# Kernel tuning notes

Measured on AMD Instinct MI355X. Metric: run time of the kernel, lower is better.

The kernel has to match this reference:

```python
import jax, jax.numpy as jnp
import numpy as np

INPUT_SIZE = 256
HIDDEN_SIZE = 128
OUTPUT_SIZE = 16
N_NODES = 100000
N_EDGES = 1600000


def setup_inputs() -> dict:
    key = jax.random.key(0)
    k_x, k_e, k_w, k_bc, k_wl, k_bl = jax.random.split(key, 6)
    x = jax.random.normal(k_x, (N_NODES, INPUT_SIZE), dtype=jnp.float32)
    edge_index = jax.random.randint(k_e, (2, N_EDGES), 0, N_NODES, dtype=jnp.int64)
    # GCNConv params: lin weight (no bias inside lin), bias added after aggregation
    s1 = 1.0 / np.sqrt(INPUT_SIZE)
    W_conv = jax.random.uniform(k_w, (INPUT_SIZE, HIDDEN_SIZE), jnp.float32, -s1, s1)
    b_conv = jnp.zeros((HIDDEN_SIZE,), jnp.float32)
    s2 = 1.0 / np.sqrt(HIDDEN_SIZE)
    W_lin = jax.random.uniform(k_wl, (HIDDEN_SIZE, OUTPUT_SIZE), jnp.float32, -s2, s2)
    b_lin = jax.random.uniform(k_bl, (OUTPUT_SIZE,), jnp.float32, -s2, s2)
    return {"x": x, "edge_index": edge_index, "W_conv": W_conv, "b_conv": b_conv,
            "W_lin": W_lin, "b_lin": b_lin}


def reference(x, edge_index, W_conv, b_conv, W_lin, b_lin):
    N = x.shape[0]
    # GCNConv: add self-loops, symmetric degree normalization, scatter-add aggregation
    loop = jnp.arange(N, dtype=edge_index.dtype)
    src = jnp.concatenate([edge_index[0], loop])  # [E+N]
    dst = jnp.concatenate([edge_index[1], loop])  # [E+N]
    deg = jax.ops.segment_sum(jnp.ones_like(dst, dtype=x.dtype), dst, num_segments=N)
    dinv = jnp.where(deg > 0, jax.lax.rsqrt(deg), 0.0)
    norm = dinv[src] * dinv[dst]  # [E+N]
    h = x @ W_conv  # [N, H] transform before propagation (as in PyG GCNConv)
    msgs = h[src] * norm[:, None]  # [E+N, H] gathered messages
    agg = jax.ops.segment_sum(msgs, dst, num_segments=N) + b_conv  # [N, H]
    h = jax.nn.relu(agg)
    # dropout is identity in eval mode
    logits = h @ W_lin + b_lin  # [N, C]
    return jax.nn.log_softmax(logits, axis=1)
```

## Files before the change

kernel.cpp:

```cpp
#include <hip/hip_runtime.h>
#include <math.h>

#define NN    100000
#define INF_  256
#define HID   128
#define OUTF  16
#define NE    1600000
#define BUK   256
#define NBUK  ((NN + BUK - 1) / BUK)
#define NB_F  128
#define EPB_F (NE / NB_F)
#define NB2   (NBUK * NB_F)
#define WPREP_B 128
#define GEMM_B ((NN + 127) / 128)
#define GBLK  3125
#define NPW   8

typedef __attribute__((ext_vector_type(4))) float f32x4;
typedef __attribute__((ext_vector_type(8))) short bf16x8;

__device__ inline unsigned short f32_to_bf16(float f) {
  union { float f; unsigned int u; } v; v.f = f;
  unsigned int x = v.u;
  unsigned int r = x + 0x7fffu + ((x >> 16) & 1u);
  return (unsigned short)(r >> 16);
}
__device__ inline unsigned pack_bf16(float f0, float f1) {
  return (unsigned)f32_to_bf16(f0) | ((unsigned)f32_to_bf16(f1) << 16);
}
__device__ inline float bf16lo_to_f32(unsigned int u) {
  union { unsigned int u; float f; } v; v.u = u << 16; return v.f;
}
__device__ inline float bf16hi_to_f32(unsigned int u) {
  union { unsigned int u; float f; } v; v.u = u & 0xffff0000u; return v.f;
}

#define ACC_FP8(u, acc) do { \
  acc[0] += __builtin_amdgcn_cvt_f32_fp8((u).x, 0); \
  acc[1] += __builtin_amdgcn_cvt_f32_fp8((u).x, 1); \
  acc[2] += __builtin_amdgcn_cvt_f32_fp8((u).x, 2); \
  acc[3] += __builtin_amdgcn_cvt_f32_fp8((u).x, 3); \
  acc[4] += __builtin_amdgcn_cvt_f32_fp8((u).y, 0); \
  acc[5] += __builtin_amdgcn_cvt_f32_fp8((u).y, 1); \
  acc[6] += __builtin_amdgcn_cvt_f32_fp8((u).y, 2); \
  acc[7] += __builtin_amdgcn_cvt_f32_fp8((u).y, 3); \
} while (0)

__global__ __launch_bounds__(256) void k_pre(const int* __restrict__ dst,
                                             int* __restrict__ H,
                                             const float* __restrict__ W,
                                             unsigned short* __restrict__ WTs) {
  __shared__ int lh[NBUK];
  const int t = threadIdx.x;
  if (blockIdx.x < NB_F) {
    const int b = blockIdx.x;
    for (int i = t; i < NBUK; i += 256) lh[i] = 0;
    __syncthreads();
    const int beg = b * EPB_F;
    for (int i = beg + t; i < beg + EPB_F; i += 256) atomicAdd(&lh[dst[i] >> 8], 1);
    __syncthreads();
    for (int i = t; i < NBUK; i += 256) H[i * NB_F + b] = lh[i];
  } else {
    const int i = (blockIdx.x - NB_F) * 256 + t;
    if (i < INF_ * HID) {
      const int k = i >> 7, n = i & 127;
      const int s = k >> 5, c = (k >> 3) & 3, j = k & 7;
      const int chunk = s * 512 + n * 4 + (c ^ (n & 3));
      WTs[chunk * 8 + j] = f32_to_bf16(W[i]);
    }
  }
}

__global__ __launch_bounds__(256) void k_fillb(const int* __restrict__ src,
                                               const int* __restrict__ dst,
                                               const int* __restrict__ H,
                                               int* __restrict__ gB,
                                               unsigned int* __restrict__ binned) {
  __shared__ int lbase[NBUK];
  __shared__ int lcnt[NBUK];
  __shared__ int tot[NBUK];
  __shared__ int bb[NBUK + 1];
  __shared__ int sh[256];
  const int t = threadIdx.x;
  const int myblk = blockIdx.x;

#pragma unroll
  for (int rr = 0; rr < 2; ++rr) {
    const int i = t + rr * 256;
    if (i < NBUK) {
      const int* row = &H[i * NB_F];
      int pre = 0, tt = 0;
      for (int k = 0; k < NB_F; ++k) {
        const int h = row[k];
        tt += h;
        if (k < myblk) pre += h;
      }
      tot[i] = tt; lbase[i] = pre; lcnt[i] = 0;
    }
  }
  __syncthreads();
  const int i0 = 2 * t, i1 = 2 * t + 1;
  const int va = (i0 < NBUK) ? tot[i0] : 0;
  const int vb = (i1 < NBUK) ? tot[i1] : 0;
  sh[t] = va + vb;
  __syncthreads();
  for (int off = 1; off < 256; off <<= 1) {
    int tmp = (t >= off) ? sh[t - off] : 0;
    __syncthreads();
    sh[t] += tmp;
    __syncthreads();
  }
  int run = (t > 0) ? sh[t - 1] : 0;
  if (i0 < NBUK) bb[i0] = run;
  if (i1 < NBUK) bb[i1] = run + va;
  if (t == 255) bb[NBUK] = run + va + vb;
  __syncthreads();
#pragma unroll
  for (int rr = 0; rr < 2; ++rr) {
    const int i = t + rr * 256;
    if (i < NBUK) {
      lbase[i] += bb[i];
      if (myblk == 0) gB[i] = bb[i];
    }
  }
  if (myblk == 0 && t == 0) gB[NBUK] = bb[NBUK];
  __syncthreads();

  const int beg = myblk * EPB_F;
#pragma unroll 4
  for (int i = beg + t; i < beg + EPB_F; i += 256) {
    const int d = dst[i];
    const int b = d >> 8;
    const unsigned w = ((unsigned)src[i] << 8) | (unsigned)(d & 255);
    const int pos = atomicAdd(&lcnt[b], 1);
    binned[lbase[b] + pos] = w;
  }
}

__global__ __launch_bounds__(256) void k_csr(const unsigned int* __restrict__ binned,
                                             const int* __restrict__ gB,
                                             int* __restrict__ rowptr,
                                             float* __restrict__ dinv,
                                             int* __restrict__ csr) {
  __shared__ int hist[BUK];
  __shared__ int sh[256];
  __shared__ int lcur[BUK];
  const int b = blockIdx.x, t = threadIdx.x;
  hist[t] = 0;
  __syncthreads();
  const int e0 = gB[b], e1 = gB[b + 1];
  for (int i = e0 + t; i < e1; i += 256) atomicAdd(&hist[binned[i] & 255u], 1);
  __syncthreads();
  const int hv = hist[t];
  sh[t] = hv;
  __syncthreads();
  for (int off = 1; off < 256; off <<= 1) {
    int tmp = (t >= off) ? sh[t - off] : 0;
    __syncthreads();
    sh[t] += tmp;
    __syncthreads();
  }
  const int excl = sh[t] - hv;
  lcur[t] = excl;
  const int nid = b * BUK + t;
  if (nid < NN) {
    rowptr[nid] = e0 + excl;
    dinv[nid] = rsqrtf((float)(hv + 1));
  }
  if (b == NBUK - 1 && t == 0) rowptr[NN] = e1;
  __syncthreads();
  for (int i = e0 + t; i < e1; i += 256) {
    const unsigned w = binned[i];
    const int pos = atomicAdd(&lcur[w & 255u], 1);
    csr[e0 + pos] = (int)(w >> 8);
  }
}

__global__ __launch_bounds__(256) void k_gemm(const float* __restrict__ x,
                                              const unsigned short* __restrict__ WTs,
                                              const float* __restrict__ dinv,
                                              uint4* __restrict__ h2b4,
                                              uint2* __restrict__ h8) {
  __shared__ unsigned short xs[128 * 32];
  __shared__ unsigned short ws[128 * 32];
  const int tid = threadIdx.x;
  const int wave = tid >> 6, lane = tid & 63;
  const int l15 = lane & 15, l4 = lane >> 4;
  const int row0 = blockIdx.x * 128;

  f32x4 acc[2][8];
#pragma unroll
  for (int rb = 0; rb < 2; ++rb)
#pragma unroll
    for (int n = 0; n < 8; ++n) { acc[rb][n].x = 0.f; acc[rb][n].y = 0.f; acc[rb][n].z = 0.f; acc[rb][n].w = 0.f; }

  for (int s = 0; s < 8; ++s) {
#pragma unroll
    for (int p = 0; p < 2; ++p) {
      const int c = tid + p * 256;
      const int row = c >> 2, kc = c & 3;
      const int grow = row0 + row;
      unsigned short tmp[8];
      if (grow < NN) {
        const float4 v0 = *(const float4*)&x[(size_t)grow * INF_ + s * 32 + kc * 8];
        const float4 v1 = *(const float4*)&x[(size_t)grow * INF_ + s * 32 + kc * 8 + 4];
        tmp[0] = f32_to_bf16(v0.x); tmp[1] = f32_to_bf16(v0.y);
        tmp[2] = f32_to_bf16(v0.z); tmp[3] = f32_to_bf16(v0.w);
        tmp[4] = f32_to_bf16(v1.x); tmp[5] = f32_to_bf16(v1.y);
        tmp[6] = f32_to_bf16(v1.z); tmp[7] = f32_to_bf16(v1.w);
      } else {
#pragma unroll
        for (int j = 0; j < 8; ++j) tmp[j] = 0;
      }
      const int phys = kc ^ (row & 3);
      *(bf16x8*)&xs[(row * 4 + phys) * 8] = *(bf16x8*)tmp;
    }
#pragma unroll
    for (int p = 0; p < 2; ++p) {
      const int c = tid + p * 256;
      *(bf16x8*)&ws[c * 8] = *(const bf16x8*)&WTs[(s * 512 + c) * 8];
    }
    __syncthreads();
    bf16x8 af[2];
#pragma unroll
    for (int rb = 0; rb < 2; ++rb) {
      const int row = wave * 32 + rb * 16 + l15;
      af[rb] = *(const bf16x8*)&xs[(row * 4 + (l4 ^ (row & 3))) * 8];
    }
#pragma unroll
    for (int n = 0; n < 8; ++n) {
      const int col = n * 16 + l15;
      const bf16x8 bf = *(const bf16x8*)&ws[(col * 4 + (l4 ^ (col & 3))) * 8];
      acc[0][n] = __builtin_amdgcn_mfma_f32_16x16x32_bf16(af[0], bf, acc[0][n], 0, 0, 0);
      acc[1][n] = __builtin_amdgcn_mfma_f32_16x16x32_bf16(af[1], bf, acc[1][n], 0, 0, 0);
    }
    __syncthreads();
  }
#pragma unroll
  for (int rb = 0; rb < 2; ++rb) {
#pragma unroll
    for (int r = 0; r < 4; ++r) {
      const int rowg = row0 + wave * 32 + rb * 16 + l4 * 4 + r;
      if (rowg < NN) {
        const float dv = dinv[rowg];
        float vv[8];
#pragma unroll
        for (int n = 0; n < 8; ++n) vv[n] = acc[rb][n][r] * dv;
        uint4 o4;
        o4.x = pack_bf16(vv[0], vv[1]);
        o4.y = pack_bf16(vv[2], vv[3]);
        o4.z = pack_bf16(vv[4], vv[5]);
        o4.w = pack_bf16(vv[6], vv[7]);
        h2b4[(size_t)rowg * 16 + l15] = o4;
        int a0 = 0, a1 = 0;
        a0 = __builtin_amdgcn_cvt_pk_fp8_f32(vv[0], vv[1], a0, false);
        a0 = __builtin_amdgcn_cvt_pk_fp8_f32(vv[2], vv[3], a0, true);
        a1 = __builtin_amdgcn_cvt_pk_fp8_f32(vv[4], vv[5], a1, false);
        a1 = __builtin_amdgcn_cvt_pk_fp8_f32(vv[6], vv[7], a1, true);
        h8[(size_t)rowg * 16 + l15] = make_uint2((unsigned)a0, (unsigned)a1);
      }
    }
  }
}

__global__ __launch_bounds__(256) void k_gather(const int* __restrict__ rowptr,
                                                const int* __restrict__ csr,
                                                const uint2* __restrict__ h8p,
                                                const uint4* __restrict__ h2b4,
                                                const float* __restrict__ dinv,
                                                const float* __restrict__ bc,
                                                const float* __restrict__ Wl,
                                                const float* __restrict__ bl,
                                                float* __restrict__ out) {
  const int lane = threadIdx.x & 63;
  const int m = lane & 15, eg = lane >> 4;
  const int wid = __builtin_amdgcn_readfirstlane(blockIdx.x * 4 + (threadIdx.x >> 6));
  const int v0 = wid * NPW;
  if (v0 >= NN) return;
  const int v1 = min(v0 + NPW, NN);

  float4 wl[8];
#pragma unroll
  for (int r = 0; r < 8; ++r) wl[r] = *(const float4*)&Wl[(size_t)(16 * r + m) * OUTF + 4 * eg];
  float bcj[8];
#pragma unroll
  for (int j = 0; j < 8; ++j) bcj[j] = bc[16 * j + m];
  const float4 bl4 = *(const float4*)&bl[4 * eg];

  for (int v = v0; v < v1; ++v) {
    const int rp = __builtin_amdgcn_readfirstlane(rowptr[v]);
    const int re = __builtin_amdgcn_readfirstlane(rowptr[v + 1]);
    float acc[8];
#pragma unroll
    for (int q = 0; q < 8; ++q) acc[q] = 0.f;

    for (int base = rp; base < re; base += 64) {
      const int nb = min(64, re - base);
      const int csrv = (base + lane < re) ? csr[base + lane] : 0;
      int o = 0;
      for (; o + 32 <= nb; o += 32) {
        const int s0 = __shfl(csrv, o + eg);
        const int s1 = __shfl(csrv, o + 4 + eg);
        const int s2 = __shfl(csrv, o + 8 + eg);
        const int s3 = __shfl(csrv, o + 12 + eg);
        const int s4 = __shfl(csrv, o + 16 + eg);
        const int s5 = __shfl(csrv, o + 20 + eg);
        const int s6 = __shfl(csrv, o + 24 + eg);
        const int s7 = __shfl(csrv, o + 28 + eg);
        const uint2 u0 = h8p[(size_t)s0 * 16 + m];
        const uint2 u1 = h8p[(size_t)s1 * 16 + m];
        const uint2 u2 = h8p[(size_t)s2 * 16 + m];
        const uint2 u3 = h8p[(size_t)s3 * 16 + m];
        const uint2 u4 = h8p[(size_t)s4 * 16 + m];
        const uint2 u5 = h8p[(size_t)s5 * 16 + m];
        const uint2 u6 = h8p[(size_t)s6 * 16 + m];
        const uint2 u7 = h8p[(size_t)s7 * 16 + m];
        ACC_FP8(u0, acc); ACC_FP8(u1, acc); ACC_FP8(u2, acc); ACC_FP8(u3, acc);
        ACC_FP8(u4, acc); ACC_FP8(u5, acc); ACC_FP8(u6, acc); ACC_FP8(u7, acc);
      }
      for (; o + 16 <= nb; o += 16) {
        const int s0 = __shfl(csrv, o + eg);
        const int s1 = __shfl(csrv, o + 4 + eg);
        const int s2 = __shfl(csrv, o + 8 + eg);
        const int s3 = __shfl(csrv, o + 12 + eg);
        const uint2 u0 = h8p[(size_t)s0 * 16 + m];
        const uint2 u1 = h8p[(size_t)s1 * 16 + m];
        const uint2 u2 = h8p[(size_t)s2 * 16 + m];
        const uint2 u3 = h8p[(size_t)s3 * 16 + m];
        ACC_FP8(u0, acc); ACC_FP8(u1, acc); ACC_FP8(u2, acc); ACC_FP8(u3, acc);
      }
      for (; o < nb; o += 4) {
        const int src = __shfl(csrv, o + eg);
        if (o + eg < nb) {
          const uint2 u = h8p[(size_t)src * 16 + m];
          ACC_FP8(u, acc);
        }
      }
    }
#pragma unroll
    for (int q = 0; q < 8; ++q) {
      acc[q] += __shfl_xor(acc[q], 16);
      acc[q] += __shfl_xor(acc[q], 32);
    }
    const float dv = dinv[v];
    const uint4 su = h2b4[(size_t)v * 16 + m];
    float t[8];
    t[0] = fmaxf(fmaf(dv, acc[0] + bf16lo_to_f32(su.x), bcj[0]), 0.f);
    t[1] = fmaxf(fmaf(dv, acc[1] + bf16hi_to_f32(su.x), bcj[1]), 0.f);
    t[2] = fmaxf(fmaf(dv, acc[2] + bf16lo_to_f32(su.y), bcj[2]), 0.f);
    t[3] = fmaxf(fmaf(dv, acc[3] + bf16hi_to_f32(su.y), bcj[3]), 0.f);
    t[4] = fmaxf(fmaf(dv, acc[4] + bf16lo_to_f32(su.z), bcj[4]), 0.f);
    t[5] = fmaxf(fmaf(dv, acc[5] + bf16hi_to_f32(su.z), bcj[5]), 0.f);
    t[6] = fmaxf(fmaf(dv, acc[6] + bf16lo_to_f32(su.w), bcj[6]), 0.f);
    t[7] = fmaxf(fmaf(dv, acc[7] + bf16hi_to_f32(su.w), bcj[7]), 0.f);
    float p0 = 0.f, p1 = 0.f, p2 = 0.f, p3 = 0.f;
#pragma unroll
    for (int r = 0; r < 8; ++r) {
      p0 = fmaf(t[r], wl[r].x, p0);
      p1 = fmaf(t[r], wl[r].y, p1);
      p2 = fmaf(t[r], wl[r].z, p2);
      p3 = fmaf(t[r], wl[r].w, p3);
    }
#pragma unroll
    for (int off = 1; off <= 8; off <<= 1) {
      p0 += __shfl_xor(p0, off);
      p1 += __shfl_xor(p1, off);
      p2 += __shfl_xor(p2, off);
      p3 += __shfl_xor(p3, off);
    }
    p0 += bl4.x; p1 += bl4.y; p2 += bl4.z; p3 += bl4.w;
    float mx = fmaxf(fmaxf(p0, p1), fmaxf(p2, p3));
    mx = fmaxf(mx, __shfl_xor(mx, 16));
    mx = fmaxf(mx, __shfl_xor(mx, 32));
    float se = expf(p0 - mx) + expf(p1 - mx) + expf(p2 - mx) + expf(p3 - mx);
    se += __shfl_xor(se, 16);
    se += __shfl_xor(se, 32);
    const float lse = mx + logf(se);
    if (m == 0) {
      float4 o4;
      o4.x = p0 - lse; o4.y = p1 - lse; o4.z = p2 - lse; o4.w = p3 - lse;
      *(float4*)&out[(size_t)v * OUTF + 4 * eg] = o4;
    }
  }
}

extern "C" void kernel_launch(void* const* d_in, const int* in_sizes, int n_in,
                              void* d_out, int out_size, void* d_ws, size_t ws_size,
                              hipStream_t stream) {
  const float* x  = (const float*)d_in[0];
  const int*   ei = (const int*)d_in[1];
  const float* Wc = (const float*)d_in[2];
  const float* bc = (const float*)d_in[3];
  const float* Wl = (const float*)d_in[4];
  const float* bl = (const float*)d_in[5];
  float* out = (float*)d_out;

  uint4* h2b4 = (uint4*)d_ws;
  unsigned short* WTs = (unsigned short*)(h2b4 + (size_t)NN * 16);
  float* dinv   = (float*)(WTs + (size_t)INF_ * HID);
  int*   rowptr = (int*)(dinv + NN);
  int*   H      = rowptr + NN + 1;
  int*   gB     = H + NB2;
  unsigned int* binned = (unsigned int*)(gB + NBUK + 1);
  int*   csr    = (int*)(binned + NE);
  uint2* h8     = (uint2*)(csr + NE);

  const int* srcv = ei;
  const int* dstv = ei + NE;

  k_pre<<<NB_F + WPREP_B, 256, 0, stream>>>(dstv, H, Wc, WTs);
  k_fillb<<<NB_F, 256, 0, stream>>>(srcv, dstv, H, gB, binned);
  k_csr<<<NBUK, 256, 0, stream>>>(binned, gB, rowptr, dinv, csr);
  k_gemm<<<GEMM_B, 256, 0, stream>>>(x, WTs, dinv, h2b4, h8);
  k_gather<<<GBLK, 256, 0, stream>>>(rowptr, csr, h8, h2b4, dinv, bc, Wl, bl, out);
}
```

Baseline: 196.5 us.

## Split FP8 feature table into column slices for cache-resident gather, add merge kernel

The GEMM now writes the FP8 hidden features as four 32-column slices stored as separate planes. Each slice is 3.2MB and can stay resident in L2/LLC while blocks mapped to that slice gather from it. The gather kernel is restructured so each block handles one slice and writes fp32 partial sums to a workspace. A new merge kernel applies the normalization, bias, ReLU, the small linear layer and log-softmax through shared memory. The self-loop term now uses the FP8 value instead of the bf16 copy, which lowers precision slightly. The change adds a 51MB fp32 intermediate write and read plus one extra kernel launch, in exchange for better cache locality of the random gathers.

```diff
diff --git a/kernel.cpp b/kernel.cpp
--- a/kernel.cpp
+++ b/kernel.cpp
@@ -13,8 +13,8 @@
 #define NB2   (NBUK * NB_F)
 #define WPREP_B 128
 #define GEMM_B ((NN + 127) / 128)
-#define GBLK  3125
-#define NPW   8
+#define NRANGE ((NN + 63) / 64)
+#define GW_BLOCKS 2048
 
 typedef __attribute__((ext_vector_type(4))) float f32x4;
 typedef __attribute__((ext_vector_type(8))) short bf16x8;
@@ -25,26 +25,19 @@
   unsigned int r = x + 0x7fffu + ((x >> 16) & 1u);
   return (unsigned short)(r >> 16);
 }
-__device__ inline unsigned pack_bf16(float f0, float f1) {
-  return (unsigned)f32_to_bf16(f0) | ((unsigned)f32_to_bf16(f1) << 16);
-}
-__device__ inline float bf16lo_to_f32(unsigned int u) {
-  union { unsigned int u; float f; } v; v.u = u << 16; return v.f;
-}
-__device__ inline float bf16hi_to_f32(unsigned int u) {
-  union { unsigned int u; float f; } v; v.u = u & 0xffff0000u; return v.f;
-}
-
-#define ACC_FP8(u, acc) do { \
-  acc[0] += __builtin_amdgcn_cvt_f32_fp8((u).x, 0); \
-  acc[1] += __builtin_amdgcn_cvt_f32_fp8((u).x, 1); \
-  acc[2] += __builtin_amdgcn_cvt_f32_fp8((u).x, 2); \
-  acc[3] += __builtin_amdgcn_cvt_f32_fp8((u).x, 3); \
-  acc[4] += __builtin_amdgcn_cvt_f32_fp8((u).y, 0); \
-  acc[5] += __builtin_amdgcn_cvt_f32_fp8((u).y, 1); \
-  acc[6] += __builtin_amdgcn_cvt_f32_fp8((u).y, 2); \
-  acc[7] += __builtin_amdgcn_cvt_f32_fp8((u).y, 3); \
+
+#define ACC4(u) do { \
+  a0 += __builtin_amdgcn_cvt_f32_fp8((u), 0); \
+  a1 += __builtin_amdgcn_cvt_f32_fp8((u), 1); \
+  a2 += __builtin_amdgcn_cvt_f32_fp8((u), 2); \
+  a3 += __builtin_amdgcn_cvt_f32_fp8((u), 3); \
 } while (0)
+
+__device__ inline int chmap(int c_lin) {
+  const int s = c_lin >> 5, g = (c_lin >> 2) & 7, k = c_lin & 3;
+  const int kk = (k == 0) ? 0 : (k == 1) ? 16 : (k == 2) ? 1 : 17;
+  return 32 * s + 2 * g + kk;
+}
 
 __global__ __launch_bounds__(256) void k_pre(const int* __restrict__ dst,
                                              int* __restrict__ H,
@@ -179,8 +172,7 @@
 __global__ __launch_bounds__(256) void k_gemm(const float* __restrict__ x,
                                               const unsigned short* __restrict__ WTs,
                                               const float* __restrict__ dinv,
-                                              uint4* __restrict__ h2b4,
-                                              uint2* __restrict__ h8) {
+                                              unsigned short* __restrict__ h8q) {
   __shared__ unsigned short xs[128 * 32];
   __shared__ unsigned short ws[128 * 32];
   const int tid = threadIdx.x;
@@ -246,141 +238,147 @@
         float vv[8];
 #pragma unroll
         for (int n = 0; n < 8; ++n) vv[n] = acc[rb][n][r] * dv;
-        uint4 o4;
-        o4.x = pack_bf16(vv[0], vv[1]);
-        o4.y = pack_bf16(vv[2], vv[3]);
-        o4.z = pack_bf16(vv[4], vv[5]);
-        o4.w = pack_bf16(vv[6], vv[7]);
-        h2b4[(size_t)rowg * 16 + l15] = o4;
-        int a0 = 0, a1 = 0;
-        a0 = __builtin_amdgcn_cvt_pk_fp8_f32(vv[0], vv[1], a0, false);
-        a0 = __builtin_amdgcn_cvt_pk_fp8_f32(vv[2], vv[3], a0, true);
-        a1 = __builtin_amdgcn_cvt_pk_fp8_f32(vv[4], vv[5], a1, false);
-        a1 = __builtin_amdgcn_cvt_pk_fp8_f32(vv[6], vv[7], a1, true);
-        h8[(size_t)rowg * 16 + l15] = make_uint2((unsigned)a0, (unsigned)a1);
-      }
-    }
-  }
-}
-
-__global__ __launch_bounds__(256) void k_gather(const int* __restrict__ rowptr,
-                                                const int* __restrict__ csr,
-                                                const uint2* __restrict__ h8p,
-                                                const uint4* __restrict__ h2b4,
-                                                const float* __restrict__ dinv,
-                                                const float* __restrict__ bc,
-                                                const float* __restrict__ Wl,
-                                                const float* __restrict__ bl,
-                                                float* __restrict__ out) {
+#pragma unroll
+        for (int s2 = 0; s2 < 4; ++s2) {
+          const int aa = __builtin_amdgcn_cvt_pk_fp8_f32(vv[2 * s2], vv[2 * s2 + 1], 0, false);
+          h8q[(size_t)s2 * NN * 16 + (size_t)rowg * 16 + l15] = (unsigned short)aa;
+        }
+      }
+    }
+  }
+}
+
+__global__ __launch_bounds__(256) void k_gath(const int* __restrict__ rowptr,
+                                              const int* __restrict__ csr,
+                                              const unsigned int* __restrict__ h8q,
+                                              float* __restrict__ sums) {
   const int lane = threadIdx.x & 63;
-  const int m = lane & 15, eg = lane >> 4;
-  const int wid = __builtin_amdgcn_readfirstlane(blockIdx.x * 4 + (threadIdx.x >> 6));
-  const int v0 = wid * NPW;
-  if (v0 >= NN) return;
-  const int v1 = min(v0 + NPW, NN);
-
-  float4 wl[8];
-#pragma unroll
-  for (int r = 0; r < 8; ++r) wl[r] = *(const float4*)&Wl[(size_t)(16 * r + m) * OUTF + 4 * eg];
-  float bcj[8];
-#pragma unroll
-  for (int j = 0; j < 8; ++j) bcj[j] = bc[16 * j + m];
-  const float4 bl4 = *(const float4*)&bl[4 * eg];
-
-  for (int v = v0; v < v1; ++v) {
-    const int rp = __builtin_amdgcn_readfirstlane(rowptr[v]);
-    const int re = __builtin_amdgcn_readfirstlane(rowptr[v + 1]);
-    float acc[8];
-#pragma unroll
-    for (int q = 0; q < 8; ++q) acc[q] = 0.f;
-
-    for (int base = rp; base < re; base += 64) {
-      const int nb = min(64, re - base);
-      const int csrv = (base + lane < re) ? csr[base + lane] : 0;
-      int o = 0;
-      for (; o + 32 <= nb; o += 32) {
-        const int s0 = __shfl(csrv, o + eg);
-        const int s1 = __shfl(csrv, o + 4 + eg);
-        const int s2 = __shfl(csrv, o + 8 + eg);
-        const int s3 = __shfl(csrv, o + 12 + eg);
-        const int s4 = __shfl(csrv, o + 16 + eg);
-        const int s5 = __shfl(csrv, o + 20 + eg);
-        const int s6 = __shfl(csrv, o + 24 + eg);
-        const int s7 = __shfl(csrv, o + 28 + eg);
-        const uint2 u0 = h8p[(size_t)s0 * 16 + m];
-        const uint2 u1 = h8p[(size_t)s1 * 16 + m];
-        const uint2 u2 = h8p[(size_t)s2 * 16 + m];
-        const uint2 u3 = h8p[(size_t)s3 * 16 + m];
-        const uint2 u4 = h8p[(size_t)s4 * 16 + m];
-        const uint2 u5 = h8p[(size_t)s5 * 16 + m];
-        const uint2 u6 = h8p[(size_t)s6 * 16 + m];
-        const uint2 u7 = h8p[(size_t)s7 * 16 + m];
-        ACC_FP8(u0, acc); ACC_FP8(u1, acc); ACC_FP8(u2, acc); ACC_FP8(u3, acc);
-        ACC_FP8(u4, acc); ACC_FP8(u5, acc); ACC_FP8(u6, acc); ACC_FP8(u7, acc);
-      }
-      for (; o + 16 <= nb; o += 16) {
-        const int s0 = __shfl(csrv, o + eg);
-        const int s1 = __shfl(csrv, o + 4 + eg);
-        const int s2 = __shfl(csrv, o + 8 + eg);
-        const int s3 = __shfl(csrv, o + 12 + eg);
-        const uint2 u0 = h8p[(size_t)s0 * 16 + m];
-        const uint2 u1 = h8p[(size_t)s1 * 16 + m];
-        const uint2 u2 = h8p[(size_t)s2 * 16 + m];
-        const uint2 u3 = h8p[(size_t)s3 * 16 + m];
-        ACC_FP8(u0, acc); ACC_FP8(u1, acc); ACC_FP8(u2, acc); ACC_FP8(u3, acc);
-      }
-      for (; o < nb; o += 4) {
-        const int src = __shfl(csrv, o + eg);
-        if (o + eg < nb) {
-          const uint2 u = h8p[(size_t)src * 16 + m];
-          ACC_FP8(u, acc);
+  const int w = threadIdx.x >> 6;
+  const int g = lane & 7, eg = lane >> 3;
+  const int x = blockIdx.x & 7;
+  const int s = x & 3;
+  const int worker = ((x >> 2) << 8) + (blockIdx.x >> 3);
+  const unsigned* hs = h8q + (size_t)s * NN * 8;
+
+  for (int r = worker; r < NRANGE; r += 512) {
+    const int vbase = r * 64 + w * 16;
+    for (int i = 0; i < 16; ++i) {
+      const int v = vbase + i;
+      if (v >= NN) break;
+      const int rp = __builtin_amdgcn_readfirstlane(rowptr[v]);
+      const int re = __builtin_amdgcn_readfirstlane(rowptr[v + 1]);
+      float a0 = 0.f, a1 = 0.f, a2 = 0.f, a3 = 0.f;
+
+      for (int base = rp; base < re; base += 64) {
+        const int nb = min(64, re - base);
+        int csrv = 0;
+        if (base + lane < re) csrv = __builtin_nontemporal_load(&csr[base + lane]);
+        int o = 0;
+        for (; o + 32 <= nb; o += 32) {
+          const int s0 = __shfl(csrv, o + eg);
+          const int s1 = __shfl(csrv, o + 8 + eg);
+          const int s2 = __shfl(csrv, o + 16 + eg);
+          const int s3 = __shfl(csrv, o + 24 + eg);
+          const unsigned u0 = hs[(size_t)s0 * 8 + g];
+          const unsigned u1 = hs[(size_t)s1 * 8 + g];
+          const unsigned u2 = hs[(size_t)s2 * 8 + g];
+          const unsigned u3 = hs[(size_t)s3 * 8 + g];
+          ACC4(u0); ACC4(u1); ACC4(u2); ACC4(u3);
         }
-      }
-    }
-#pragma unroll
-    for (int q = 0; q < 8; ++q) {
-      acc[q] += __shfl_xor(acc[q], 16);
-      acc[q] += __shfl_xor(acc[q], 32);
-    }
-    const float dv = dinv[v];
-    const uint4 su = h2b4[(size_t)v * 16 + m];
-    float t[8];
-    t[0] = fmaxf(fmaf(dv, acc[0] + bf16lo_to_f32(su.x), bcj[0]), 0.f);
-    t[1] = fmaxf(fmaf(dv, acc[1] + bf16hi_to_f32(su.x), bcj[1]), 0.f);
-    t[2] = fmaxf(fmaf(dv, acc[2] + bf16lo_to_f32(su.y), bcj[2]), 0.f);
-    t[3] = fmaxf(fmaf(dv, acc[3] + bf16hi_to_f32(su.y), bcj[3]), 0.f);
-    t[4] = fmaxf(fmaf(dv, acc[4] + bf16lo_to_f32(su.z), bcj[4]), 0.f);
-    t[5] = fmaxf(fmaf(dv, acc[5] + bf16hi_to_f32(su.z), bcj[5]), 0.f);
-    t[6] = fmaxf(fmaf(dv, acc[6] + bf16lo_to_f32(su.w), bcj[6]), 0.f);
-    t[7] = fmaxf(fmaf(dv, acc[7] + bf16hi_to_f32(su.w), bcj[7]), 0.f);
-    float p0 = 0.f, p1 = 0.f, p2 = 0.f, p3 = 0.f;
-#pragma unroll
-    for (int r = 0; r < 8; ++r) {
-      p0 = fmaf(t[r], wl[r].x, p0);
-      p1 = fmaf(t[r], wl[r].y, p1);
-      p2 = fmaf(t[r], wl[r].z, p2);
-      p3 = fmaf(t[r], wl[r].w, p3);
-    }
-#pragma unroll
-    for (int off = 1; off <= 8; off <<= 1) {
-      p0 += __shfl_xor(p0, off);
-      p1 += __shfl_xor(p1, off);
-      p2 += __shfl_xor(p2, off);
-      p3 += __shfl_xor(p3, off);
-    }
-    p0 += bl4.x; p1 += bl4.y; p2 += bl4.z; p3 += bl4.w;
-    float mx = fmaxf(fmaxf(p0, p1), fmaxf(p2, p3));
-    mx = fmaxf(mx, __shfl_xor(mx, 16));
-    mx = fmaxf(mx, __shfl_xor(mx, 32));
-    float se = expf(p0 - mx) + expf(p1 - mx) + expf(p2 - mx) + expf(p3 - mx);
-    se += __shfl_xor(se, 16);
-    se += __shfl_xor(se, 32);
-    const float lse = mx + logf(se);
-    if (m == 0) {
-      float4 o4;
-      o4.x = p0 - lse; o4.y = p1 - lse; o4.z = p2 - lse; o4.w = p3 - lse;
-      *(float4*)&out[(size_t)v * OUTF + 4 * eg] = o4;
-    }
+        for (; o < nb; o += 8) {
+          const int slot = o + eg;
+          const int sv = __shfl(csrv, slot);
+          if (slot < nb) {
+            const unsigned u = hs[(size_t)sv * 8 + g];
+            ACC4(u);
+          }
+        }
+      }
+      {
+        const unsigned u = hs[(size_t)v * 8 + g];
+        if (eg == 0) ACC4(u);
+      }
+      a0 += __shfl_xor(a0, 8);  a0 += __shfl_xor(a0, 16); a0 += __shfl_xor(a0, 32);
+      a1 += __shfl_xor(a1, 8);  a1 += __shfl_xor(a1, 16); a1 += __shfl_xor(a1, 32);
+      a2 += __shfl_xor(a2, 8);  a2 += __shfl_xor(a2, 16); a2 += __shfl_xor(a2, 32);
+      a3 += __shfl_xor(a3, 8);  a3 += __shfl_xor(a3, 16); a3 += __shfl_xor(a3, 32);
+      if (eg == 0) {
+        f32x4 o4;
+        o4.x = a0; o4.y = a1; o4.z = a2; o4.w = a3;
+        __builtin_nontemporal_store(o4, (f32x4*)&sums[(size_t)v * HID + s * 32 + g * 4]);
+      }
+    }
+  }
+}
+
+__global__ __launch_bounds__(256) void k_merge(const float* __restrict__ sums,
+                                               const float* __restrict__ dinv,
+                                               const float* __restrict__ bc,
+                                               const float* __restrict__ Wl,
+                                               const float* __restrict__ bl,
+                                               float* __restrict__ out) {
+  __shared__ float tL[64 * 132];
+  __shared__ float WlL[HID * OUTF];
+  __shared__ float bcL[HID];
+  __shared__ float blL[OUTF];
+  const int t = threadIdx.x;
+  const int v0 = blockIdx.x * 64;
+
+  {
+    const int c = t >> 1, half = (t & 1) * 8;
+    const int mc = chmap(c);
+    const float4* srcw = (const float4*)&Wl[(size_t)mc * OUTF + half];
+    float4* dstw = (float4*)&WlL[c * OUTF + half];
+    dstw[0] = srcw[0];
+    dstw[1] = srcw[1];
+  }
+  if (t < HID) bcL[t] = bc[chmap(t)];
+  if (t < OUTF) blL[t] = bl[t];
+  __syncthreads();
+
+#pragma unroll
+  for (int i = 0; i < 8; ++i) {
+    const int e4 = i * 256 + t;
+    const int nl = e4 >> 5, c4 = e4 & 31;
+    const int v = v0 + nl;
+    f32x4 tv = {0.f, 0.f, 0.f, 0.f};
+    if (v < NN) {
+      const f32x4 sv = __builtin_nontemporal_load((const f32x4*)&sums[(size_t)v * HID + c4 * 4]);
+      const float dv = dinv[v];
+      tv.x = fmaxf(fmaf(dv, sv.x, bcL[c4 * 4 + 0]), 0.f);
+      tv.y = fmaxf(fmaf(dv, sv.y, bcL[c4 * 4 + 1]), 0.f);
+      tv.z = fmaxf(fmaf(dv, sv.z, bcL[c4 * 4 + 2]), 0.f);
+      tv.w = fmaxf(fmaf(dv, sv.w, bcL[c4 * 4 + 3]), 0.f);
+    }
+    *(f32x4*)&tL[nl * 132 + c4 * 4] = tv;
+  }
+  __syncthreads();
+
+  const int nl = t >> 2, q = t & 3;
+  const int v = v0 + nl;
+  const float* tp = &tL[nl * 132];
+  float a0 = 0.f, a1 = 0.f, a2 = 0.f, a3 = 0.f;
+#pragma unroll 8
+  for (int c = 0; c < HID; ++c) {
+    const float tc = tp[c];
+    const float4 w4 = *(const float4*)&WlL[c * OUTF + 4 * q];
+    a0 = fmaf(tc, w4.x, a0);
+    a1 = fmaf(tc, w4.y, a1);
+    a2 = fmaf(tc, w4.z, a2);
+    a3 = fmaf(tc, w4.w, a3);
+  }
+  a0 += blL[4 * q + 0]; a1 += blL[4 * q + 1]; a2 += blL[4 * q + 2]; a3 += blL[4 * q + 3];
+  float mx = fmaxf(fmaxf(a0, a1), fmaxf(a2, a3));
+  mx = fmaxf(mx, __shfl_xor(mx, 1));
+  mx = fmaxf(mx, __shfl_xor(mx, 2));
+  float se = expf(a0 - mx) + expf(a1 - mx) + expf(a2 - mx) + expf(a3 - mx);
+  se += __shfl_xor(se, 1);
+  se += __shfl_xor(se, 2);
+  const float lse = mx + logf(se);
+  if (v < NN) {
+    float4 o4;
+    o4.x = a0 - lse; o4.y = a1 - lse; o4.z = a2 - lse; o4.w = a3 - lse;
+    *(float4*)&out[(size_t)v * OUTF + 4 * q] = o4;
   }
 }
 
@@ -395,15 +393,15 @@
   const float* bl = (const float*)d_in[5];
   float* out = (float*)d_out;
 
-  uint4* h2b4 = (uint4*)d_ws;
-  unsigned short* WTs = (unsigned short*)(h2b4 + (size_t)NN * 16);
+  float* sums = (float*)d_ws;
+  unsigned short* WTs = (unsigned short*)(sums + (size_t)NN * HID);
   float* dinv   = (float*)(WTs + (size_t)INF_ * HID);
   int*   rowptr = (int*)(dinv + NN);
   int*   H      = rowptr + NN + 1;
   int*   gB     = H + NB2;
   unsigned int* binned = (unsigned int*)(gB + NBUK + 1);
   int*   csr    = (int*)(binned + NE);
-  uint2* h8     = (uint2*)(csr + NE);
+  unsigned short* h8q = (unsigned short*)(csr + NE);
 
   const int* srcv = ei;
   const int* dstv = ei + NE;
@@ -411,6 +409,7 @@
   k_pre<<<NB_F + WPREP_B, 256, 0, stream>>>(dstv, H, Wc, WTs);
   k_fillb<<<NB_F, 256, 0, stream>>>(srcv, dstv, H, gB, binned);
   k_csr<<<NBUK, 256, 0, stream>>>(binned, gB, rowptr, dinv, csr);
-  k_gemm<<<GEMM_B, 256, 0, stream>>>(x, WTs, dinv, h2b4, h8);
-  k_gather<<<GBLK, 256, 0, stream>>>(rowptr, csr, h8, h2b4, dinv, bc, Wl, bl, out);
-}
+  k_gemm<<<GEMM_B, 256, 0, stream>>>(x, WTs, dinv, h8q);
+  k_gath<<<GW_BLOCKS, 256, 0, stream>>>(rowptr, csr, (const unsigned int*)h8q, sums);
+  k_merge<<<NRANGE, 256, 0, stream>>>(sums, dinv, bc, Wl, bl, out);
+}
```

After: 260.4 us. 1.33x slower.
